# Kernel tuning notes

Hardware: AMD Instinct MI355X
Metric: run time of the kernel (lower is better)

The kernel has to match this reference:

```python
import jax, jax.numpy as jnp
import numpy as np

B, T, U1, D, V = 4, 256, 65, 512, 1024

def setup_inputs() -> dict:
    key = jax.random.key(0)
    k1, k2, k3 = jax.random.split(key, 3)
    encoder_outputs = jax.random.normal(k1, (B, T, D), dtype=jnp.float32)
    decoder_outputs = jax.random.normal(k2, (B, U1, D), dtype=jnp.float32)
    # nn.Linear(2D, V, bias=False): weight shape (V, 2D), scaled like torch default init
    fc_weight = jax.random.normal(k3, (V, 2 * D), dtype=jnp.float32) * (1.0 / np.sqrt(2 * D))
    return {"encoder_outputs": encoder_outputs, "decoder_outputs": decoder_outputs, "fc_weight": fc_weight}

def reference(encoder_outputs, decoder_outputs, fc_weight):
    # Original: expand enc->(B,T,U,D), dec->(B,T,U,D), cat -> (B,T,U,2D), GELU(tanh), Linear.
    # Since GELU is elementwise and the linear has no bias, this equals two small
    # projections broadcast-added over the (T,U) grid (identical math, fused form).
    De = encoder_outputs.shape[-1]
    ge = jax.nn.gelu(encoder_outputs, approximate=True)  # (B,T,De)
    gd = jax.nn.gelu(decoder_outputs, approximate=True)  # (B,U,Dd)
    enc_proj = jnp.einsum('btd,vd->btv', ge, fc_weight[:, :De])  # (B,T,V)
    dec_proj = jnp.einsum('bud,vd->buv', gd, fc_weight[:, De:])  # (B,U,V)
    return enc_proj[:, :, None, :] + dec_proj[:, None, :, :]      # (B,T,U,V)
```

## Files before the change

kernel.cpp:

```cpp
#include <hip/hip_runtime.h>
#include <hip/hip_bf16.h>


#define B_ 4
#define T_ 256
#define U_ 65
#define D_ 512
#define V_ 1024

typedef __attribute__((ext_vector_type(8))) short bf16x8;
typedef __attribute__((ext_vector_type(4))) float f32x4;

__device__ __forceinline__ float gelu_tanh(float x) {
    const float c = 0.7978845608028654f;
    float x3 = x * x * x;
    float t = tanhf(c * (x + 0.044715f * x3));
    return 0.5f * x * (1.0f + t);
}

__global__ __launch_bounds__(256)
void prep_kernel(const float* __restrict__ enc,
                 const float* __restrict__ dec,
                 const float* __restrict__ W,
                 __hip_bfloat16* __restrict__ geB,
                 __hip_bfloat16* __restrict__ gdB,
                 __hip_bfloat16* __restrict__ WB) {
    const int NE4 = (B_ * T_ * D_) / 4;
    const int ND4 = (B_ * U_ * D_) / 4;
    const int NW4 = (V_ * 2 * D_) / 4;
    int i = blockIdx.x * blockDim.x + threadIdx.x;
    if (i < NE4) {
        float4 v = ((const float4*)enc)[i];
        __hip_bfloat16* p = geB + i * 4;
        p[0] = __float2bfloat16(gelu_tanh(v.x));
        p[1] = __float2bfloat16(gelu_tanh(v.y));
        p[2] = __float2bfloat16(gelu_tanh(v.z));
        p[3] = __float2bfloat16(gelu_tanh(v.w));
    } else if (i < NE4 + ND4) {
        int j = i - NE4;
        float4 v = ((const float4*)dec)[j];
        __hip_bfloat16* p = gdB + j * 4;
        p[0] = __float2bfloat16(gelu_tanh(v.x));
        p[1] = __float2bfloat16(gelu_tanh(v.y));
        p[2] = __float2bfloat16(gelu_tanh(v.z));
        p[3] = __float2bfloat16(gelu_tanh(v.w));
    } else if (i < NE4 + ND4 + NW4) {
        int j = i - NE4 - ND4;
        float4 v = ((const float4*)W)[j];
        __hip_bfloat16* p = WB + j * 4;
        p[0] = __float2bfloat16(v.x);
        p[1] = __float2bfloat16(v.y);
        p[2] = __float2bfloat16(v.z);
        p[3] = __float2bfloat16(v.w);
    }
}

__global__ __launch_bounds__(256)
void gemm_kernel(const __hip_bfloat16* __restrict__ geB,
                 const __hip_bfloat16* __restrict__ gdB,
                 const __hip_bfloat16* __restrict__ WB,
                 float* __restrict__ encP,
                 float* __restrict__ decP) {
    int blk = blockIdx.x;
    const __hip_bfloat16* A;
    float* C;
    int M, kofs, mt, nt;
    if (blk < 256) {
        A = geB; C = encP; M = B_ * T_; kofs = 0;
        mt = blk >> 4; nt = blk & 15;
    } else {
        blk -= 256;
        A = gdB; C = decP; M = B_ * U_; kofs = D_;
        mt = blk >> 4; nt = blk & 15;
    }
    const int lane = threadIdx.x & 63;
    const int w    = threadIdx.x >> 6;
    const int wr   = w >> 1, wc = w & 1;
    const int r16  = lane & 15;
    const int k8   = (lane >> 4) * 8;

    const int m_base = mt * 64 + wr * 32;
    const int n_base = nt * 64 + wc * 32;

    f32x4 acc[2][2] = {};
    for (int k0 = 0; k0 < D_; k0 += 32) {
        bf16x8 a[2], b[2];
#pragma unroll
        for (int mi = 0; mi < 2; ++mi) {
            int row = m_base + mi * 16 + r16;
            int rr = row < M ? row : 0;
            a[mi] = *(const bf16x8*)(A + (size_t)rr * D_ + k0 + k8);
        }
#pragma unroll
        for (int ni = 0; ni < 2; ++ni) {
            int col = n_base + ni * 16 + r16;
            b[ni] = *(const bf16x8*)(WB + (size_t)col * (2 * D_) + kofs + k0 + k8);
        }
#pragma unroll
        for (int mi = 0; mi < 2; ++mi)
#pragma unroll
            for (int ni = 0; ni < 2; ++ni)
                acc[mi][ni] = __builtin_amdgcn_mfma_f32_16x16x32_bf16(
                    a[mi], b[ni], acc[mi][ni], 0, 0, 0);
    }
    const int c_row0 = (lane >> 4) * 4;
#pragma unroll
    for (int mi = 0; mi < 2; ++mi) {
#pragma unroll
        for (int j = 0; j < 4; ++j) {
            int row = m_base + mi * 16 + c_row0 + j;
            if (row < M) {
#pragma unroll
                for (int ni = 0; ni < 2; ++ni) {
                    int col = n_base + ni * 16 + r16;
                    C[(size_t)row * V_ + col] = acc[mi][ni][j];
                }
            }
        }
    }
}

__global__ __launch_bounds__(256)
void bcast_kernel(const float* __restrict__ encP,
                  const float* __restrict__ decP,
                  float* __restrict__ out) {
    const int NROWS = B_ * T_ * U_;
    const int tid = threadIdx.x;
    for (int n = blockIdx.x; n < NROWS; n += gridDim.x) {
        int bt = n / U_;
        int u  = n - bt * U_;
        int b  = bt >> 8;
        const float4* e4 = (const float4*)(encP + (size_t)bt * V_);
        const float4* d4 = (const float4*)(decP + ((size_t)b * U_ + u) * V_);
        float4* o4 = (float4*)(out + (size_t)n * V_);
        float4 ev = e4[tid];
        float4 dv = d4[tid];
        float4 ov;
        ov.x = ev.x + dv.x;
        ov.y = ev.y + dv.y;
        ov.z = ev.z + dv.z;
        ov.w = ev.w + dv.w;
        o4[tid] = ov;
    }
}

extern "C" void kernel_launch(void* const* d_in, const int* in_sizes, int n_in,
                              void* d_out, int out_size, void* d_ws, size_t ws_size,
                              hipStream_t stream) {
    const float* enc = (const float*)d_in[0];
    const float* dec = (const float*)d_in[1];
    const float* W   = (const float*)d_in[2];
    float* out = (float*)d_out;

    char* ws = (char*)d_ws;
    __hip_bfloat16* geB  = (__hip_bfloat16*)(ws);
    __hip_bfloat16* gdB  = (__hip_bfloat16*)(ws + 0x100000);
    __hip_bfloat16* WB   = (__hip_bfloat16*)(ws + 0x180000);
    float*          encP = (float*)(ws + 0x380000);
    float*          decP = (float*)(ws + 0x780000);

    const int total4 = (B_ * T_ * D_ + B_ * U_ * D_ + V_ * 2 * D_) / 4;
    prep_kernel<<<(total4 + 255) / 256, 256, 0, stream>>>(enc, dec, W, geB, gdB, WB);
    gemm_kernel<<<256 + 80, 256, 0, stream>>>(geB, gdB, WB, encP, decP);
    bcast_kernel<<<2048, 256, 0, stream>>>(encP, decP, out);
}
```

Before: 79.19 us.

## Reuse encoder rows in registers across all U in broadcast kernel

The broadcast-add kernel now has each block own TB=4 consecutive (b,t) rows. The encoder projection vectors stay in registers while the block loops over all U decoder rows, so each decoder row load feeds four output rows. The per-row divide and modulo go away and input reads drop. The grid becomes 256 blocks of 256 threads instead of a 2048-block grid-stride loop, which may reduce parallelism for this store-bound output.

```diff
diff --git a/kernel.cpp b/kernel.cpp
--- a/kernel.cpp
+++ b/kernel.cpp
@@ -7,6 +7,7 @@
 #define U_ 65
 #define D_ 512
 #define V_ 1024
+#define TB 4
 
 typedef __attribute__((ext_vector_type(8))) short bf16x8;
 typedef __attribute__((ext_vector_type(4))) float f32x4;
@@ -124,23 +125,29 @@
 void bcast_kernel(const float* __restrict__ encP,
                   const float* __restrict__ decP,
                   float* __restrict__ out) {
-    const int NROWS = B_ * T_ * U_;
     const int tid = threadIdx.x;
-    for (int n = blockIdx.x; n < NROWS; n += gridDim.x) {
-        int bt = n / U_;
-        int u  = n - bt * U_;
-        int b  = bt >> 8;
-        const float4* e4 = (const float4*)(encP + (size_t)bt * V_);
-        const float4* d4 = (const float4*)(decP + ((size_t)b * U_ + u) * V_);
-        float4* o4 = (float4*)(out + (size_t)n * V_);
-        float4 ev = e4[tid];
-        float4 dv = d4[tid];
-        float4 ov;
-        ov.x = ev.x + dv.x;
-        ov.y = ev.y + dv.y;
-        ov.z = ev.z + dv.z;
-        ov.w = ev.w + dv.w;
-        o4[tid] = ov;
+    const int bt0 = blockIdx.x * TB;
+    const int b   = bt0 >> 8;
+
+    float4 ev[TB];
+#pragma unroll
+    for (int i = 0; i < TB; ++i)
+        ev[i] = ((const float4*)(encP + (size_t)(bt0 + i) * V_))[tid];
+
+    const float4* d4 = (const float4*)(decP + (size_t)b * U_ * V_);
+    float4* o4 = (float4*)(out + (size_t)bt0 * U_ * V_);
+
+    for (int u = 0; u < U_; ++u) {
+        float4 dv = d4[(size_t)u * (V_ / 4) + tid];
+#pragma unroll
+        for (int i = 0; i < TB; ++i) {
+            float4 ov;
+            ov.x = ev[i].x + dv.x;
+            ov.y = ev[i].y + dv.y;
+            ov.z = ev[i].z + dv.z;
+            ov.w = ev[i].w + dv.w;
+            o4[((size_t)i * U_ + u) * (V_ / 4) + tid] = ov;
+        }
     }
 }
 
@@ -162,5 +169,5 @@
     const int total4 = (B_ * T_ * D_ + B_ * U_ * D_ + V_ * 2 * D_) / 4;
     prep_kernel<<<(total4 + 255) / 256, 256, 0, stream>>>(enc, dec, W, geB, gdB, WB);
     gemm_kernel<<<256 + 80, 256, 0, stream>>>(geB, gdB, WB, encP, decP);
-    bcast_kernel<<<2048, 256, 0, stream>>>(encP, decP, out);
+    bcast_kernel<<<(B_ * T_) / TB, 256, 0, stream>>>(encP, decP, out);
 }
```

After: 116.5 us. 1.47x slower.
